# Kernel optimization log

Measured on AMD Instinct MI355X. Metric: run time of the kernel, lower is better.

The kernel has to match this reference:

```python
import jax, jax.numpy as jnp
import numpy as np

N, D, E, TOP_K = 16384, 1024, 8, 2

def setup_inputs() -> dict:
    key = jax.random.key(0)
    ks = jax.random.split(key, 8)
    sc = 1.0 / np.sqrt(D)
    return {
        "x": jax.random.normal(ks[0], (N, D), dtype=jnp.float32),
        "context_vector": jax.random.uniform(ks[1], (E,), dtype=jnp.float32),
        "router_w": jax.random.uniform(ks[2], (E, D), minval=-sc, maxval=sc),
        "router_b": jax.random.uniform(ks[3], (E,), minval=-sc, maxval=sc),
        "expert_w": jax.random.uniform(ks[4], (E, D, D), minval=-sc, maxval=sc),
        "expert_b": jax.random.uniform(ks[5], (E, D), minval=-sc, maxval=sc),
        "context_weight": jax.random.uniform(ks[6], (1,), dtype=jnp.float32),
    }

def reference(x, context_vector, router_w, router_b, expert_w, expert_b, context_weight):
    # Router: gate logits with conceptual context bias. [N, E]
    gate_logits = x @ router_w.T + router_b + context_weight * context_vector
    weights = jax.nn.softmax(gate_logits, axis=-1)

    # Top-k selection and renormalization. [N, k]
    top_k_weights, top_k_indices = jax.lax.top_k(weights, TOP_K)
    top_k_weights = top_k_weights / jnp.sum(top_k_weights, axis=-1, keepdims=True)

    # All-expert outputs (dense grouped GEMM): y[n,e,:] = x[n] @ W[e].T + b[e]
    all_out = jnp.einsum('nd,efd->nef', x, expert_w) + expert_b  # [N, E, D]

    # Gather the top-k expert outputs per token and combine. [N, k, D]
    gathered = jnp.take_along_axis(all_out, top_k_indices[:, :, None], axis=1)
    expert_outputs = jnp.sum(top_k_weights[:, :, None] * gathered, axis=1)  # [N, D]

    # Load-balancing loss: avg router prob . fraction of tokens routed per expert
    avg_router_prob = weights.mean(axis=0)  # [E]
    assignment_mask = jax.nn.one_hot(top_k_indices, E).sum(axis=1)  # [N, E]
    fraction_routed = assignment_mask.mean(axis=0)  # [E]
    load_loss = jnp.sum(avg_router_prob * fraction_routed)

    return expert_outputs, load_loss
```

## Files before the change

### kernel.cpp

```cpp
#include <hip/hip_runtime.h>
#include <stdint.h>

#define N_TOK 16384
#define DDIM  1024
#define NEXP  8
#define CNT_STRIDE 64

#define BM 256
#define BN 256
#define BK 64
#define NKT 16
#define MAX_TILES 136
#define EP_PITCH 72

typedef __bf16 bf16x8 __attribute__((ext_vector_type(8)));
typedef float  f32x4  __attribute__((ext_vector_type(4)));

__device__ __forceinline__ unsigned short f2bf(float f) {
  union { float f; uint32_t u; } a; a.f = f;
  uint32_t u = a.u;
  u += 0x7fffu + ((u >> 16) & 1u);
  return (unsigned short)(u >> 16);
}

__device__ __forceinline__ float bf2f(unsigned short u) {
  union { uint32_t u; float f; } a; a.u = ((uint32_t)u) << 16;
  return a.f;
}

__device__ __forceinline__ float2 bfpair(uint32_t u) {
  union { uint32_t u; float f; } lo, hi;
  lo.u = u << 16; hi.u = u & 0xffff0000u;
  return make_float2(lo.f, hi.f);
}

__device__ __forceinline__ void load_lds16(const void* g, void* l) {
  __builtin_amdgcn_global_load_lds(
      (const __attribute__((address_space(1))) void*)g,
      (__attribute__((address_space(3))) void*)l,
      16, 0, 0);
}

#define SCHED_FENCE() __builtin_amdgcn_sched_barrier(0)
#define BAR_PLAIN() do { SCHED_FENCE(); asm volatile("s_barrier" ::: "memory"); SCHED_FENCE(); } while (0)
#define BAR_LGKM0() do { SCHED_FENCE(); asm volatile("s_waitcnt lgkmcnt(0)\n\ts_barrier" ::: "memory"); SCHED_FENCE(); } while (0)
#define BAR_VM(N)   do { SCHED_FENCE(); asm volatile("s_waitcnt vmcnt(" #N ")\n\ts_barrier" ::: "memory"); SCHED_FENCE(); } while (0)

__global__ __launch_bounds__(512) void router_kernel(
    const float* __restrict__ x, const float* __restrict__ rw,
    const float* __restrict__ rb, const float* __restrict__ cv,
    const float* __restrict__ cwp,
    const float4* __restrict__ ew4, ushort4* __restrict__ wb4,
    unsigned short* __restrict__ xg,
    int* __restrict__ perm_idx, float* __restrict__ perm_w,
    int* __restrict__ inv_idx,
    int* __restrict__ cnt, float* __restrict__ sum_w)
{
  __shared__ int   sCnt[NEXP];
  __shared__ int   sBase[NEXP];
  __shared__ float sSW[NEXP];
  __shared__ int   sE0[32], sE1[32], sR0[32], sR1[32];
  __shared__ float sW0[32], sW1[32];

  const int tid = threadIdx.x;
  if (tid < NEXP) { sCnt[tid] = 0; sSW[tid] = 0.0f; }
  __syncthreads();

  const int wave = tid >> 6;
  const int lane = tid & 63;

  float lsw[NEXP];
#pragma unroll
  for (int e = 0; e < NEXP; ++e) lsw[e] = 0.0f;

  const float cw = cwp[0];

  for (int t = 0; t < 4; ++t) {
    const int i = wave * 4 + t;
    const int n = blockIdx.x * 32 + i;

    float p[NEXP];
#pragma unroll
    for (int e = 0; e < NEXP; ++e) p[e] = 0.0f;

    const float2* x2 = (const float2*)(x + (size_t)n * DDIM);
    uint32_t* xgp = (uint32_t*)(xg + (size_t)n * DDIM);

    float2 xv[8];
#pragma unroll
    for (int it = 0; it < 8; ++it) xv[it] = x2[lane + 64 * it];
#pragma unroll
    for (int it = 0; it < 8; ++it) {
      int dp = lane + 64 * it;
      xgp[dp] = (uint32_t)f2bf(xv[it].x) | ((uint32_t)f2bf(xv[it].y) << 16);
#pragma unroll
      for (int e = 0; e < NEXP; ++e) {
        float2 wv = ((const float2*)(rw + e * DDIM))[dp];
        p[e] = fmaf(xv[it].x, wv.x, fmaf(xv[it].y, wv.y, p[e]));
      }
    }
#pragma unroll
    for (int e = 0; e < NEXP; ++e) {
#pragma unroll
      for (int off = 32; off > 0; off >>= 1)
        p[e] += __shfl_xor(p[e], off, 64);
    }

    if (lane == 0) {
      float w[NEXP];
      float m = -1e30f;
#pragma unroll
      for (int e = 0; e < NEXP; ++e) {
        w[e] = p[e] + rb[e] + cw * cv[e];
        m = fmaxf(m, w[e]);
      }
      float s = 0.0f;
#pragma unroll
      for (int e = 0; e < NEXP; ++e) { w[e] = expf(w[e] - m); s += w[e]; }
      float inv = 1.0f / s;
#pragma unroll
      for (int e = 0; e < NEXP; ++e) { w[e] *= inv; lsw[e] += w[e]; }
      int e0 = 0;
#pragma unroll
      for (int e = 1; e < NEXP; ++e) if (w[e] > w[e0]) e0 = e;
      int e1 = (e0 == 0) ? 1 : 0;
#pragma unroll
      for (int e = 0; e < NEXP; ++e) if (e != e0 && w[e] > w[e1]) e1 = e;
      float rsum = 1.0f / (w[e0] + w[e1]);
      int r0 = atomicAdd(&sCnt[e0], 1);
      int r1 = atomicAdd(&sCnt[e1], 1);
      sE0[i] = e0; sE1[i] = e1; sR0[i] = r0; sR1[i] = r1;
      sW0[i] = w[e0] * rsum; sW1[i] = w[e1] * rsum;
    }
  }

  if (lane == 0) {
#pragma unroll
    for (int e = 0; e < NEXP; ++e) atomicAdd(&sSW[e], lsw[e]);
  }
  __syncthreads();

  if (tid < NEXP) {
    sBase[tid] = atomicAdd(&cnt[tid * CNT_STRIDE], sCnt[tid]);
    atomicAdd(&sum_w[tid * CNT_STRIDE], sSW[tid]);
  }
  __syncthreads();

  if (tid < 64) {
    int i = tid >> 1, k = tid & 1;
    int e = k ? sE1[i] : sE0[i];
    int r = k ? sR1[i] : sR0[i];
    float wv = k ? sW1[i] : sW0[i];
    int pos = sBase[e] + r;
    int n = blockIdx.x * 32 + i;
    perm_idx[e * N_TOK + pos] = n;
    perm_w [e * N_TOK + pos] = wv;
    inv_idx[2 * n + k] = (e << 14) | pos;
  }

  size_t base = (size_t)blockIdx.x * 512 + tid;
#pragma unroll
  for (int i2 = 0; i2 < 8; ++i2) {
    size_t idx = base + (size_t)i2 * 262144;
    float4 v = ew4[idx];
    wb4[idx] = make_ushort4(f2bf(v.x), f2bf(v.y), f2bf(v.z), f2bf(v.w));
  }
}

template<int MODE>
__global__ __launch_bounds__(512, 2) void moe_gemm_kernel(
    const unsigned short* __restrict__ xg, const unsigned short* __restrict__ wb,
    const float* __restrict__ eb,
    const int* __restrict__ perm_idx, const float* __restrict__ perm_w,
    const int* __restrict__ cnt,
    unsigned short* __restrict__ ybuf, float* __restrict__ out)
{
  const int id = blockIdx.x;
  const int tn = id / MAX_TILES;
  const int tileIdx = id - tn * MAX_TILES;

  int e = -1, tm = 0, count = 0, ebase = 0, pref = 0;
#pragma unroll
  for (int j = 0; j < NEXP; ++j) {
    int c = cnt[j * CNT_STRIDE];
    int t = (c + BM - 1) >> 8;
    if (e < 0 && tileIdx < pref + t) { e = j; tm = tileIdx - pref; count = c; }
    if (e < 0) ebase += c;
    pref += t;
  }
  if (e < 0) return;

  __shared__ union {
    struct { __bf16 As[2][BM * BK]; __bf16 Bs[2][BN * BK]; } g;
    __bf16 ep[8 * 64 * EP_PITCH];
  } sm;
  __shared__ int   tokS[BM];
  __shared__ float wtS[BM];

  const int tid = threadIdx.x;
  const int wave = tid >> 6;
  const int lane = tid & 63;

  if (tid < BM) {
    int row = tm * BM + tid;
    int rc = row < count ? row : count - 1;
    tokS[tid] = perm_idx[e * N_TOK + rc];
    wtS[tid] = (row < count) ? perm_w[e * N_TOK + row] : 0.0f;
  }
  __syncthreads();

  const unsigned short* wbase = wb + (size_t)e * DDIM * DDIM;
  const int rl = wave * 16 + (lane >> 3);
  const int cg = (((lane & 7) ^ (lane >> 3)) & 7) * 8;

  const unsigned short* gA[2][2];
  const unsigned short* gB[2][2];
#pragma unroll
  for (int h = 0; h < 2; ++h)
#pragma unroll
    for (int j = 0; j < 2; ++j) {
      gA[h][j] = xg + (size_t)tokS[h * 128 + rl + j * 8] * DDIM + cg;
      gB[h][j] = wbase + (size_t)(tn * BN + h * 128 + rl + j * 8) * DDIM + cg;
    }

#define STG_A(h, bsel) do { \
    load_lds16(gA[h][0], &sm.g.As[bsel][((h) * 128 + wave * 16) * BK]);     gA[h][0] += BK; \
    load_lds16(gA[h][1], &sm.g.As[bsel][((h) * 128 + wave * 16 + 8) * BK]); gA[h][1] += BK; \
  } while (0)
#define STG_B(h, bsel) do { \
    load_lds16(gB[h][0], &sm.g.Bs[bsel][((h) * 128 + wave * 16) * BK]);     gB[h][0] += BK; \
    load_lds16(gB[h][1], &sm.g.Bs[bsel][((h) * 128 + wave * 16 + 8) * BK]); gB[h][1] += BK; \
  } while (0)

  STG_A(0, 0); STG_A(1, 0); STG_B(0, 0); STG_B(1, 0);
  STG_A(0, 1);
  BAR_VM(0);

  const int wr = wave >> 2;
  const int wc = wave & 3;
  const int quad = lane >> 4;
  const int l15 = lane & 15;
  const int sl0 = (quad ^ (l15 & 7)) * 8;
  const int rowA = (wr * 128 + l15) * BK + sl0;
  const int rowB = (wc * 64 + l15) * BK + sl0;

  f32x4 acc[8][4] = {};

#pragma unroll
  for (int t = 0; t < NKT; ++t) {
    const int b = t & 1, nb = b ^ 1;
    const __bf16* Ab = sm.g.As[b];
    const __bf16* Bb = sm.g.Bs[b];
    bf16x8 Bf[4][2], Af[4][2];

    if (t + 1 < NKT) STG_A(1, nb);
#pragma unroll
    for (int ni = 0; ni < 2; ++ni)
#pragma unroll
      for (int ks = 0; ks < 2; ++ks)
        Bf[ni][ks] = *(const bf16x8*)&Bb[(rowB + ni * 1024) ^ (ks * 32)];
#pragma unroll
    for (int mi = 0; mi < 4; ++mi)
#pragma unroll
      for (int ks = 0; ks < 2; ++ks)
        Af[mi][ks] = *(const bf16x8*)&Ab[(rowA + mi * 1024) ^ (ks * 32)];
    __builtin_amdgcn_s_setprio(1);
#pragma unroll
    for (int ks = 0; ks < 2; ++ks)
#pragma unroll
      for (int mi = 0; mi < 4; ++mi)
#pragma unroll
        for (int ni = 0; ni < 2; ++ni)
          acc[mi][ni] = __builtin_amdgcn_mfma_f32_16x16x32_bf16(Bf[ni][ks], Af[mi][ks], acc[mi][ni], 0, 0, 0);
    __builtin_amdgcn_s_setprio(0);
    BAR_PLAIN();

    if (t + 1 < NKT) STG_B(0, nb);
#pragma unroll
    for (int ni = 2; ni < 4; ++ni)
#pragma unroll
      for (int ks = 0; ks < 2; ++ks)
        Bf[ni][ks] = *(const bf16x8*)&Bb[(rowB + ni * 1024) ^ (ks * 32)];
    __builtin_amdgcn_s_setprio(1);
#pragma unroll
    for (int ks = 0; ks < 2; ++ks)
#pragma unroll
      for (int mi = 0; mi < 4; ++mi)
#pragma unroll
        for (int ni = 2; ni < 4; ++ni)
          acc[mi][ni] = __builtin_amdgcn_mfma_f32_16x16x32_bf16(Bf[ni][ks], Af[mi][ks], acc[mi][ni], 0, 0, 0);
    __builtin_amdgcn_s_setprio(0);
    BAR_PLAIN();

    if (t + 1 < NKT) STG_B(1, nb);
#pragma unroll
    for (int mi = 0; mi < 4; ++mi)
#pragma unroll
      for (int ks = 0; ks < 2; ++ks)
        Af[mi][ks] = *(const bf16x8*)&Ab[(rowA + (mi + 4) * 1024) ^ (ks * 32)];
    __builtin_amdgcn_s_setprio(1);
#pragma unroll
    for (int ks = 0; ks < 2; ++ks)
#pragma unroll
      for (int mi = 0; mi < 4; ++mi)
#pragma unroll
        for (int ni = 0; ni < 2; ++ni)
          acc[mi + 4][ni] = __builtin_amdgcn_mfma_f32_16x16x32_bf16(Bf[ni][ks], Af[mi][ks], acc[mi + 4][ni], 0, 0, 0);
    __builtin_amdgcn_s_setprio(0);
    BAR_LGKM0();

    if (t + 2 < NKT) STG_A(0, b);
    __builtin_amdgcn_s_setprio(1);
#pragma unroll
    for (int ks = 0; ks < 2; ++ks)
#pragma unroll
      for (int mi = 0; mi < 4; ++mi)
#pragma unroll
        for (int ni = 2; ni < 4; ++ni)
          acc[mi + 4][ni] = __builtin_amdgcn_mfma_f32_16x16x32_bf16(Bf[ni][ks], Af[mi][ks], acc[mi + 4][ni], 0, 0, 0);
    __builtin_amdgcn_s_setprio(0);
    if (t + 2 < NKT)      BAR_VM(2);
    else if (t + 1 < NKT) BAR_VM(0);
    else                  BAR_PLAIN();
  }

#undef STG_A
#undef STG_B

  const int valid = count - tm * BM;
  const int gb = ebase + tm * BM;

  if (MODE == 1) {
    __bf16* slab = &sm.ep[wave * (64 * EP_PITCH)];
#pragma unroll
    for (int p = 0; p < 2; ++p) {
#pragma unroll
      for (int mi4 = 0; mi4 < 4; ++mi4) {
        const int mi = p * 4 + mi4;
        float wt = wtS[wr * 128 + mi * 16 + l15];
#pragma unroll
        for (int ni = 0; ni < 4; ++ni) {
          int gcol = tn * BN + wc * 64 + ni * 16 + quad * 4;
          const float4 bv = *(const float4*)&eb[e * DDIM + gcol];
          ushort4 pk;
          pk.x = f2bf((acc[mi][ni][0] + bv.x) * wt);
          pk.y = f2bf((acc[mi][ni][1] + bv.y) * wt);
          pk.z = f2bf((acc[mi][ni][2] + bv.z) * wt);
          pk.w = f2bf((acc[mi][ni][3] + bv.w) * wt);
          *(ushort4*)&slab[(mi4 * 16 + l15) * EP_PITCH + ni * 16 + quad * 4] = pk;
        }
      }
#pragma unroll
      for (int s = 0; s < 8; ++s) {
        int lrow = s * 8 + (lane >> 3);
        uint4 v = *(const uint4*)&slab[lrow * EP_PITCH + (lane & 7) * 8];
        int brow = wr * 128 + p * 64 + lrow;
        if (brow < valid)
          *(uint4*)&ybuf[(size_t)(gb + brow) * DDIM + tn * BN + wc * 64 + (lane & 7) * 8] = v;
      }
    }
  } else {
#pragma unroll
    for (int mi = 0; mi < 8; ++mi) {
      int brow = wr * 128 + mi * 16 + l15;
      float wt = wtS[brow];
      int tok = tokS[brow];
      if (brow < valid) {
#pragma unroll
        for (int ni = 0; ni < 4; ++ni) {
          int gcol = tn * BN + wc * 64 + ni * 16 + quad * 4;
          const float4 bv = *(const float4*)&eb[e * DDIM + gcol];
          atomicAdd(out + (size_t)tok * DDIM + gcol + 0, (acc[mi][ni][0] + bv.x) * wt);
          atomicAdd(out + (size_t)tok * DDIM + gcol + 1, (acc[mi][ni][1] + bv.y) * wt);
          atomicAdd(out + (size_t)tok * DDIM + gcol + 2, (acc[mi][ni][2] + bv.z) * wt);
          atomicAdd(out + (size_t)tok * DDIM + gcol + 3, (acc[mi][ni][3] + bv.w) * wt);
        }
      }
    }
  }
}

__global__ __launch_bounds__(256) void combine_kernel(
    const unsigned short* __restrict__ ybuf, const int* __restrict__ inv_idx,
    const int* __restrict__ cnt, float* __restrict__ out)
{
  const int wave = threadIdx.x >> 6;
  const int lane = threadIdx.x & 63;
  const int n = blockIdx.x * 4 + wave;

  int base[NEXP];
  int acc = 0;
#pragma unroll
  for (int j = 0; j < NEXP; ++j) { base[j] = acc; acc += cnt[j * CNT_STRIDE]; }

  int i0 = inv_idx[2 * n];
  int i1 = inv_idx[2 * n + 1];
  int g0 = base[i0 >> 14] + (i0 & 16383);
  int g1 = base[i1 >> 14] + (i1 & 16383);

  const uint4* r0 = (const uint4*)(ybuf + (size_t)g0 * DDIM);
  const uint4* r1 = (const uint4*)(ybuf + (size_t)g1 * DDIM);
  float4* o = (float4*)(out + (size_t)n * DDIM);

#pragma unroll
  for (int it = 0; it < 2; ++it) {
    int c = lane + 64 * it;
    uint4 a = r0[c];
    uint4 b = r1[c];
    float2 a0 = bfpair(a.x), a1 = bfpair(a.y), a2 = bfpair(a.z), a3 = bfpair(a.w);
    float2 b0 = bfpair(b.x), b1 = bfpair(b.y), b2 = bfpair(b.z), b3 = bfpair(b.w);
    float4 v0, v1;
    v0.x = a0.x + b0.x; v0.y = a0.y + b0.y; v0.z = a1.x + b1.x; v0.w = a1.y + b1.y;
    v1.x = a2.x + b2.x; v1.y = a2.y + b2.y; v1.z = a3.x + b3.x; v1.w = a3.y + b3.y;
    o[2 * c] = v0;
    o[2 * c + 1] = v1;
  }
}

__global__ void loss_kernel(const float* __restrict__ sum_w,
                            const int* __restrict__ cnt,
                            float* __restrict__ out) {
  if (threadIdx.x == 0 && blockIdx.x == 0) {
    float l = 0.0f;
#pragma unroll
    for (int e = 0; e < NEXP; ++e)
      l += sum_w[e * CNT_STRIDE] * (float)cnt[e * CNT_STRIDE];
    out[(size_t)N_TOK * DDIM] = l * (1.0f / ((float)N_TOK * (float)N_TOK));
  }
}

extern "C" void kernel_launch(void* const* d_in, const int* in_sizes, int n_in,
                              void* d_out, int out_size, void* d_ws, size_t ws_size,
                              hipStream_t stream) {
  const float* x  = (const float*)d_in[0];
  const float* cv = (const float*)d_in[1];
  const float* rw = (const float*)d_in[2];
  const float* rb = (const float*)d_in[3];
  const float* ew = (const float*)d_in[4];
  const float* eb = (const float*)d_in[5];
  const float* cw = (const float*)d_in[6];
  float* out = (float*)d_out;

  char* ws = (char*)d_ws;
  unsigned short* xg = (unsigned short*)ws;
  unsigned short* wb = (unsigned short*)(ws + 33554432);
  int*   perm_idx = (int*)  (ws + 50331648);
  float* perm_w   = (float*)(ws + 50855936);
  int*   inv_idx  = (int*)  (ws + 51380224);
  int*   cnt      = (int*)  (ws + 51511296);
  float* sum_w    = (float*)(ws + 51513344);
  unsigned short* ybuf = (unsigned short*)(ws + 51515392);
  const size_t NEED = 51515392ull + 67108864ull;

  const bool big = ws_size >= NEED;

  hipMemsetAsync(cnt, 0, 4096, stream);
  if (!big)
    hipMemsetAsync(d_out, 0, (size_t)N_TOK * DDIM * sizeof(float), stream);

  router_kernel<<<N_TOK / 32, 512, 0, stream>>>(x, rw, rb, cv, cw,
                                                (const float4*)ew, (ushort4*)wb,
                                                xg, perm_idx, perm_w, inv_idx, cnt, sum_w);

  if (big) {
    moe_gemm_kernel<1><<<MAX_TILES * 4, 512, 0, stream>>>(
        xg, wb, eb, perm_idx, perm_w, cnt, ybuf, out);
    combine_kernel<<<N_TOK / 4, 256, 0, stream>>>(ybuf, inv_idx, cnt, out);
  } else {
    moe_gemm_kernel<0><<<MAX_TILES * 4, 512, 0, stream>>>(
        xg, wb, eb, perm_idx, perm_w, cnt, ybuf, out);
  }

  loss_kernel<<<1, 64, 0, stream>>>(sum_w, cnt, out);
}
```

Measured before the change: 305.9 us.

## Replace phased interleaved GEMM main loop with simple double-buffered loop

Drops the hand-interleaved four-phase main loop, which spread the next tile's global-to-LDS loads between MFMA groups with partial vmcnt waits and setprio hints. The new loop issues every load for the next tile at the top, runs all MFMAs for the current tile, then waits on vmcnt(0) and a barrier. This cuts barriers per k-tile from four to one and simplifies scheduling. In exchange it loses the fine-grained overlap and the priority boosts, and each iteration now stalls on a full drain of outstanding loads.

```diff
diff --git a/kernel.cpp b/kernel.cpp
--- a/kernel.cpp
+++ b/kernel.cpp
@@ -43,8 +43,7 @@
 
 #define SCHED_FENCE() __builtin_amdgcn_sched_barrier(0)
 #define BAR_PLAIN() do { SCHED_FENCE(); asm volatile("s_barrier" ::: "memory"); SCHED_FENCE(); } while (0)
-#define BAR_LGKM0() do { SCHED_FENCE(); asm volatile("s_waitcnt lgkmcnt(0)\n\ts_barrier" ::: "memory"); SCHED_FENCE(); } while (0)
-#define BAR_VM(N)   do { SCHED_FENCE(); asm volatile("s_waitcnt vmcnt(" #N ")\n\ts_barrier" ::: "memory"); SCHED_FENCE(); } while (0)
+#define BAR_VM0()   do { SCHED_FENCE(); asm volatile("s_waitcnt vmcnt(0)\n\ts_barrier" ::: "memory"); SCHED_FENCE(); } while (0)
 
 __global__ __launch_bounds__(512) void router_kernel(
     const float* __restrict__ x, const float* __restrict__ rw,
@@ -233,8 +232,7 @@
   } while (0)
 
   STG_A(0, 0); STG_A(1, 0); STG_B(0, 0); STG_B(1, 0);
-  STG_A(0, 1);
-  BAR_VM(0);
+  BAR_VM0();
 
   const int wr = wave >> 2;
   const int wc = wave & 3;
@@ -251,77 +249,29 @@
     const int b = t & 1, nb = b ^ 1;
     const __bf16* Ab = sm.g.As[b];
     const __bf16* Bb = sm.g.Bs[b];
-    bf16x8 Bf[4][2], Af[4][2];
-
-    if (t + 1 < NKT) STG_A(1, nb);
-#pragma unroll
-    for (int ni = 0; ni < 2; ++ni)
+
+    if (t + 1 < NKT) { STG_A(0, nb); STG_A(1, nb); STG_B(0, nb); STG_B(1, nb); }
+
+    bf16x8 Bf[4][2];
+#pragma unroll
+    for (int ni = 0; ni < 4; ++ni)
 #pragma unroll
       for (int ks = 0; ks < 2; ++ks)
         Bf[ni][ks] = *(const bf16x8*)&Bb[(rowB + ni * 1024) ^ (ks * 32)];
-#pragma unroll
-    for (int mi = 0; mi < 4; ++mi)
-#pragma unroll
-      for (int ks = 0; ks < 2; ++ks)
-        Af[mi][ks] = *(const bf16x8*)&Ab[(rowA + mi * 1024) ^ (ks * 32)];
-    __builtin_amdgcn_s_setprio(1);
-#pragma unroll
-    for (int ks = 0; ks < 2; ++ks)
-#pragma unroll
-      for (int mi = 0; mi < 4; ++mi)
-#pragma unroll
-        for (int ni = 0; ni < 2; ++ni)
-          acc[mi][ni] = __builtin_amdgcn_mfma_f32_16x16x32_bf16(Bf[ni][ks], Af[mi][ks], acc[mi][ni], 0, 0, 0);
-    __builtin_amdgcn_s_setprio(0);
-    BAR_PLAIN();
-
-    if (t + 1 < NKT) STG_B(0, nb);
-#pragma unroll
-    for (int ni = 2; ni < 4; ++ni)
-#pragma unroll
-      for (int ks = 0; ks < 2; ++ks)
-        Bf[ni][ks] = *(const bf16x8*)&Bb[(rowB + ni * 1024) ^ (ks * 32)];
-    __builtin_amdgcn_s_setprio(1);
-#pragma unroll
-    for (int ks = 0; ks < 2; ++ks)
-#pragma unroll
-      for (int mi = 0; mi < 4; ++mi)
-#pragma unroll
-        for (int ni = 2; ni < 4; ++ni)
-          acc[mi][ni] = __builtin_amdgcn_mfma_f32_16x16x32_bf16(Bf[ni][ks], Af[mi][ks], acc[mi][ni], 0, 0, 0);
-    __builtin_amdgcn_s_setprio(0);
-    BAR_PLAIN();
-
-    if (t + 1 < NKT) STG_B(1, nb);
-#pragma unroll
-    for (int mi = 0; mi < 4; ++mi)
-#pragma unroll
-      for (int ks = 0; ks < 2; ++ks)
-        Af[mi][ks] = *(const bf16x8*)&Ab[(rowA + (mi + 4) * 1024) ^ (ks * 32)];
-    __builtin_amdgcn_s_setprio(1);
-#pragma unroll
-    for (int ks = 0; ks < 2; ++ks)
-#pragma unroll
-      for (int mi = 0; mi < 4; ++mi)
-#pragma unroll
-        for (int ni = 0; ni < 2; ++ni)
-          acc[mi + 4][ni] = __builtin_amdgcn_mfma_f32_16x16x32_bf16(Bf[ni][ks], Af[mi][ks], acc[mi + 4][ni], 0, 0, 0);
-    __builtin_amdgcn_s_setprio(0);
-    BAR_LGKM0();
-
-    if (t + 2 < NKT) STG_A(0, b);
-    __builtin_amdgcn_s_setprio(1);
-#pragma unroll
-    for (int ks = 0; ks < 2; ++ks)
-#pragma unroll
-      for (int mi = 0; mi < 4; ++mi)
-#pragma unroll
-        for (int ni = 2; ni < 4; ++ni)
-          acc[mi + 4][ni] = __builtin_amdgcn_mfma_f32_16x16x32_bf16(Bf[ni][ks], Af[mi][ks], acc[mi + 4][ni], 0, 0, 0);
-    __builtin_amdgcn_s_setprio(0);
-    if (t + 2 < NKT)      BAR_VM(2);
-    else if (t + 1 < NKT) BAR_VM(0);
-    else                  BAR_PLAIN();
+
+#pragma unroll
+    for (int mi = 0; mi < 8; ++mi) {
+      bf16x8 a0 = *(const bf16x8*)&Ab[(rowA + mi * 1024)];
+      bf16x8 a1 = *(const bf16x8*)&Ab[(rowA + mi * 1024) ^ 32];
+#pragma unroll
+      for (int ni = 0; ni < 4; ++ni) {
+        acc[mi][ni] = __builtin_amdgcn_mfma_f32_16x16x32_bf16(Bf[ni][0], a0, acc[mi][ni], 0, 0, 0);
+        acc[mi][ni] = __builtin_amdgcn_mfma_f32_16x16x32_bf16(Bf[ni][1], a1, acc[mi][ni], 0, 0, 0);
+      }
+    }
+
+    if (t + 1 < NKT) BAR_VM0();
+    else             BAR_PLAIN();
   }
 
 #undef STG_A
```

Result: faster. 284.8 us (-6.9%).

## Restructure GEMM main loop into 4-phase ping-pong with deeper prefetch

Applied to the files above, without the earlier changes.

Reorders the LDS fragment loads and global-to-LDS staging in the expert GEMM loop so each of four MFMA phases is preceded by its own fragment reads and one staging load, with a barrier before every compute block. B fragments are split into B01/B23 and A fragments are reloaded halfway through. Prefetch now runs further ahead: two half-tiles of the next stage are issued in the prologue and the loop waits with vmcnt(4) instead of vmcnt(2). This is meant to overlap global loads with MFMA better and lower per-wave register pressure, at the cost of more barriers per iteration. It also adds a barrier between the two epilogue slab passes to fix a possible LDS reuse race.

```diff
diff --git a/kernel.cpp b/kernel.cpp
--- a/kernel.cpp
+++ b/kernel.cpp
@@ -43,7 +43,7 @@
 
 #define SCHED_FENCE() __builtin_amdgcn_sched_barrier(0)
 #define BAR_PLAIN() do { SCHED_FENCE(); asm volatile("s_barrier" ::: "memory"); SCHED_FENCE(); } while (0)
-#define BAR_LGKM0() do { SCHED_FENCE(); asm volatile("s_waitcnt lgkmcnt(0)\n\ts_barrier" ::: "memory"); SCHED_FENCE(); } while (0)
+#define BAR_VM0()   do { SCHED_FENCE(); asm volatile("s_waitcnt vmcnt(0)\n\ts_barrier" ::: "memory"); SCHED_FENCE(); } while (0)
 #define BAR_VM(N)   do { SCHED_FENCE(); asm volatile("s_waitcnt vmcnt(" #N ")\n\ts_barrier" ::: "memory"); SCHED_FENCE(); } while (0)
 
 __global__ __launch_bounds__(512) void router_kernel(
@@ -232,9 +232,9 @@
     load_lds16(gB[h][1], &sm.g.Bs[bsel][((h) * 128 + wave * 16 + 8) * BK]); gB[h][1] += BK; \
   } while (0)
 
-  STG_A(0, 0); STG_A(1, 0); STG_B(0, 0); STG_B(1, 0);
-  STG_A(0, 1);
-  BAR_VM(0);
+  STG_A(0, 0); STG_B(0, 0); STG_A(1, 0); STG_B(1, 0);
+  STG_B(0, 1); STG_A(0, 1);
+  BAR_VM(4);
 
   const int wr = wave >> 2;
   const int wc = wave & 3;
@@ -251,19 +251,38 @@
     const int b = t & 1, nb = b ^ 1;
     const __bf16* Ab = sm.g.As[b];
     const __bf16* Bb = sm.g.Bs[b];
-    bf16x8 Bf[4][2], Af[4][2];
-
+    bf16x8 Af[4][2], B01[2][2], B23[2][2];
+
+#pragma unroll
+    for (int mi = 0; mi < 4; ++mi) {
+      Af[mi][0] = *(const bf16x8*)&Ab[(rowA + mi * 1024)];
+      Af[mi][1] = *(const bf16x8*)&Ab[(rowA + mi * 1024) ^ 32];
+    }
+#pragma unroll
+    for (int ni = 0; ni < 2; ++ni) {
+      B01[ni][0] = *(const bf16x8*)&Bb[(rowB + ni * 1024)];
+      B01[ni][1] = *(const bf16x8*)&Bb[(rowB + ni * 1024) ^ 32];
+    }
+    if (t + 1 < NKT) STG_B(1, nb);
+    BAR_PLAIN();
+    __builtin_amdgcn_s_setprio(1);
+#pragma unroll
+    for (int ks = 0; ks < 2; ++ks)
+#pragma unroll
+      for (int mi = 0; mi < 4; ++mi)
+#pragma unroll
+        for (int ni = 0; ni < 2; ++ni)
+          acc[mi][ni] = __builtin_amdgcn_mfma_f32_16x16x32_bf16(B01[ni][ks], Af[mi][ks], acc[mi][ni], 0, 0, 0);
+    __builtin_amdgcn_s_setprio(0);
+    BAR_PLAIN();
+
+#pragma unroll
+    for (int ni = 0; ni < 2; ++ni) {
+      B23[ni][0] = *(const bf16x8*)&Bb[(rowB + (ni + 2) * 1024)];
+      B23[ni][1] = *(const bf16x8*)&Bb[(rowB + (ni + 2) * 1024) ^ 32];
+    }
     if (t + 1 < NKT) STG_A(1, nb);
-#pragma unroll
-    for (int ni = 0; ni < 2; ++ni)
-#pragma unroll
-      for (int ks = 0; ks < 2; ++ks)
-        Bf[ni][ks] = *(const bf16x8*)&Bb[(rowB + ni * 1024) ^ (ks * 32)];
-#pragma unroll
-    for (int mi = 0; mi < 4; ++mi)
-#pragma unroll
-      for (int ks = 0; ks < 2; ++ks)
-        Af[mi][ks] = *(const bf16x8*)&Ab[(rowA + mi * 1024) ^ (ks * 32)];
+    BAR_PLAIN();
     __builtin_amdgcn_s_setprio(1);
 #pragma unroll
     for (int ks = 0; ks < 2; ++ks)
@@ -271,33 +290,30 @@
       for (int mi = 0; mi < 4; ++mi)
 #pragma unroll
         for (int ni = 0; ni < 2; ++ni)
-          acc[mi][ni] = __builtin_amdgcn_mfma_f32_16x16x32_bf16(Bf[ni][ks], Af[mi][ks], acc[mi][ni], 0, 0, 0);
+          acc[mi][ni + 2] = __builtin_amdgcn_mfma_f32_16x16x32_bf16(B23[ni][ks], Af[mi][ks], acc[mi][ni + 2], 0, 0, 0);
     __builtin_amdgcn_s_setprio(0);
     BAR_PLAIN();
 
-    if (t + 1 < NKT) STG_B(0, nb);
-#pragma unroll
-    for (int ni = 2; ni < 4; ++ni)
-#pragma unroll
-      for (int ks = 0; ks < 2; ++ks)
-        Bf[ni][ks] = *(const bf16x8*)&Bb[(rowB + ni * 1024) ^ (ks * 32)];
+#pragma unroll
+    for (int mi = 0; mi < 4; ++mi) {
+      Af[mi][0] = *(const bf16x8*)&Ab[(rowA + (mi + 4) * 1024)];
+      Af[mi][1] = *(const bf16x8*)&Ab[(rowA + (mi + 4) * 1024) ^ 32];
+    }
+    if (t + 2 < NKT) STG_B(0, b);
+    BAR_PLAIN();
     __builtin_amdgcn_s_setprio(1);
 #pragma unroll
     for (int ks = 0; ks < 2; ++ks)
 #pragma unroll
       for (int mi = 0; mi < 4; ++mi)
 #pragma unroll
-        for (int ni = 2; ni < 4; ++ni)
-          acc[mi][ni] = __builtin_amdgcn_mfma_f32_16x16x32_bf16(Bf[ni][ks], Af[mi][ks], acc[mi][ni], 0, 0, 0);
+        for (int ni = 0; ni < 2; ++ni)
+          acc[mi + 4][ni] = __builtin_amdgcn_mfma_f32_16x16x32_bf16(B01[ni][ks], Af[mi][ks], acc[mi + 4][ni], 0, 0, 0);
     __builtin_amdgcn_s_setprio(0);
     BAR_PLAIN();
 
-    if (t + 1 < NKT) STG_B(1, nb);
-#pragma unroll
-    for (int mi = 0; mi < 4; ++mi)
-#pragma unroll
-      for (int ks = 0; ks < 2; ++ks)
-        Af[mi][ks] = *(const bf16x8*)&Ab[(rowA + (mi + 4) * 1024) ^ (ks * 32)];
+    if (t + 2 < NKT) STG_A(0, b);
+    BAR_PLAIN();
     __builtin_amdgcn_s_setprio(1);
 #pragma unroll
     for (int ks = 0; ks < 2; ++ks)
@@ -305,22 +321,10 @@
       for (int mi = 0; mi < 4; ++mi)
 #pragma unroll
         for (int ni = 0; ni < 2; ++ni)
-          acc[mi + 4][ni] = __builtin_amdgcn_mfma_f32_16x16x32_bf16(Bf[ni][ks], Af[mi][ks], acc[mi + 4][ni], 0, 0, 0);
+          acc[mi + 4][ni + 2] = __builtin_amdgcn_mfma_f32_16x16x32_bf16(B23[ni][ks], Af[mi][ks], acc[mi + 4][ni + 2], 0, 0, 0);
     __builtin_amdgcn_s_setprio(0);
-    BAR_LGKM0();
-
-    if (t + 2 < NKT) STG_A(0, b);
-    __builtin_amdgcn_s_setprio(1);
-#pragma unroll
-    for (int ks = 0; ks < 2; ++ks)
-#pragma unroll
-      for (int mi = 0; mi < 4; ++mi)
-#pragma unroll
-        for (int ni = 2; ni < 4; ++ni)
-          acc[mi + 4][ni] = __builtin_amdgcn_mfma_f32_16x16x32_bf16(Bf[ni][ks], Af[mi][ks], acc[mi + 4][ni], 0, 0, 0);
-    __builtin_amdgcn_s_setprio(0);
-    if (t + 2 < NKT)      BAR_VM(2);
-    else if (t + 1 < NKT) BAR_VM(0);
+    if (t + 2 < NKT)      BAR_VM(4);
+    else if (t + 1 < NKT) BAR_VM0();
     else                  BAR_PLAIN();
   }
 
@@ -358,6 +362,7 @@
         if (brow < valid)
           *(uint4*)&ybuf[(size_t)(gb + brow) * DDIM + tn * BN + wc * 64 + (lane & 7) * 8] = v;
       }
+      if (p == 0) BAR_PLAIN();
     }
   } else {
 #pragma unroll
```

New measurement: 309.6 us. About the same (+1.2%).
